# Performance work log

Hardware: AMD Instinct MI355X
Metric: run time of the kernel (lower is better)

The kernel has to match this reference:

```python
import jax, jax.numpy as jnp
import numpy as np
from jax import lax

NUM_COLS = 4
NUM_ROWS = 4
C = 16          # in_channels
K = 3           # kernel_size
B, H, Wd = 8, 128, 128
W_SCALE = 0.05  # keep activations stable through 16 chained ReLU convs


def setup_inputs() -> dict:
    key = jax.random.key(0)
    k1, k2 = jax.random.split(key, 2)
    x = jax.random.normal(k1, (B, C, H, Wd), dtype=jnp.float32)
    # one conv per grid cell: 3 input slots (left/below-prev/above), 3 output streams (right/up/down)
    W = jax.random.normal(k2, (NUM_COLS, NUM_ROWS, 3 * C, 3 * C, K, K), dtype=jnp.float32) * W_SCALE
    b = jnp.zeros((NUM_COLS, NUM_ROWS, 3 * C), dtype=jnp.float32)
    return {"input_tensor": x, "W": W, "b": b}


def _cell(w, bias, ins):
    # ins: list of 1..3 tensors [B, C, H, W]; zero-pad missing slots to 3*C channels
    if len(ins) < 3:
        pad_shape = (ins[0].shape[0], (3 - len(ins)) * C) + ins[0].shape[2:]
        ins = ins + [jnp.zeros(pad_shape, dtype=ins[0].dtype)]
    x = jnp.concatenate(ins, axis=1)  # [B, 3C, H, W]
    y = lax.conv_general_dilated(
        x, w, window_strides=(1, 1), padding="SAME",
        dimension_numbers=("NCHW", "OIHW", "NCHW"))
    y = jax.nn.relu(y + bias[None, :, None, None])
    right, up, down = jnp.split(y, 3, axis=1)  # each [B, C, H, W]
    return (right, up, down)


def reference(input_tensor, W, b):
    # Wavefront sweep: columns left->right, rows top->bottom.
    # outs[row] holds the (right, up, down) tuple of the most recently computed
    # cell in that row (previous column until overwritten this column).
    outs = [None] * NUM_ROWS
    for col in range(NUM_COLS):
        for row in range(NUM_ROWS):
            if col == 0:
                ins = [input_tensor] if row == 0 else [outs[row - 1][-1]]
            else:
                if row == 0:
                    ins = [outs[row][0], outs[row + 1][1]]
                elif row == NUM_ROWS - 1:
                    ins = [outs[row][0], outs[row - 1][-1]]
                else:
                    ins = [outs[row][0], outs[row + 1][1], outs[row - 1][-1]]
            outs[row] = _cell(W[col, row], b[col, row], ins)
    return outs[-1][0]
```

## Files before the change

### kernel.cpp

```cpp
#include <hip/hip_runtime.h>

#define HW    128
#define PW    130
#define NCELL 16
#define ABUF_PER_CELL 23040
#define ABUF_TOTAL (NCELL * ABUF_PER_CELL)
#define NSTREAMS 15
#define BORDER_PX 516
#define BORDER_TASKS (NSTREAMS * 8 * BORDER_PX * 2)

typedef _Float16 half8 __attribute__((ext_vector_type(8)));
typedef _Float16 half4 __attribute__((ext_vector_type(4)));
typedef float    f32x4 __attribute__((ext_vector_type(4)));

#define GLD_LDS(gp, lp) __builtin_amdgcn_global_load_lds( \
    (const __attribute__((address_space(1))) void*)(gp),  \
    (__attribute__((address_space(3))) void*)(lp), 16, 0, 0)

__global__ void prep_w_border_k(const float* __restrict__ W,
                                _Float16* __restrict__ Abuf,
                                _Float16* __restrict__ sbase) {
    int idx = blockIdx.x * 256 + threadIdx.x;
    if (idx < ABUF_TOTAL) {
        int j = idx & 7;
        int t = idx >> 3;
        int co = t % 48;   t /= 48;
        int quad = t & 3;  t >>= 2;
        int chunk = t % 5; t /= 5;
        int slot = t % 3;  t /= 3;
        int cell = t;
        int g = chunk * 4 + quad;
        float v = 0.f;
        if (g < 18) {
            int kh = g / 6, r6 = g % 6;
            int kw = r6 >> 1, cg = r6 & 1;
            int ci = slot * 16 + cg * 8 + j;
            v = W[((size_t)(cell * 48 + co) * 48 + ci) * 9 + kh * 3 + kw];
        }
        Abuf[idx] = (_Float16)v;
        return;
    }
    int t = idx - ABUF_TOTAL;
    if (t >= BORDER_TASKS) return;
    int h  = t & 1;
    int pb = t >> 1;
    int p  = pb % BORDER_PX;
    int bb = pb / BORDER_PX;
    int y, x;
    if (p < 260) {
        y = (p < 130) ? 0 : (PW - 1);
        x = p - ((p < 130) ? 0 : 130);
    } else {
        int e = p - 260;
        y = 1 + (e >> 1);
        x = (e & 1) ? (PW - 1) : 0;
    }
    half8 z = {};
    *(half8*)(sbase + (size_t)bb * (PW * PW * 16)
              + ((size_t)y * PW + x) * 16 + h * 8) = z;
}

struct CellIO {
    const _Float16* in0; const _Float16* in1; const _Float16* in2;
    const _Float16* Ac; const float* bc;
    _Float16* o0; _Float16* o1; _Float16* o2;
    float* fout;
};

template<int LIVE, int NIN, bool FIN, bool XIN>
__device__ __forceinline__ void cell_body(const CellIO& P, int b, _Float16* xh,
                                          const float* xsrc)
{
    const int tid = threadIdx.x;
    const int bx = blockIdx.x, by = blockIdx.y;
    const int x0 = bx * 16, y0 = by * 16;
    const int lane = tid & 63, wv = tid >> 6;
    const int n = lane & 15, quad = lane >> 4;
    const int py0 = wv * 4;

    if constexpr (XIN) {
        for (int task = tid; task < 288; task += 256) {
            int ci = task / 18, iy = task - (task / 18) * 18;
            float v[18];
#pragma unroll
            for (int ix = 0; ix < 18; ++ix) v[ix] = 0.f;
            int gy = y0 + iy - 1;
            if ((unsigned)gy < (unsigned)HW) {
                const float* rp = xsrc + (((size_t)b * 16 + ci) * HW + gy) * HW + x0;
                f32x4 q0 = *(const f32x4*)(rp);
                f32x4 q1 = *(const f32x4*)(rp + 4);
                f32x4 q2 = *(const f32x4*)(rp + 8);
                f32x4 q3 = *(const f32x4*)(rp + 12);
#pragma unroll
                for (int j = 0; j < 4; ++j) {
                    v[1 + j] = q0[j]; v[5 + j] = q1[j];
                    v[9 + j] = q2[j]; v[13 + j] = q3[j];
                }
                if (x0 > 0)       v[0]  = rp[-1];
                if (x0 < HW - 16) v[17] = rp[16];
            }
            int cg = ci >> 3, cj = ci & 7;
#pragma unroll
            for (int ix = 0; ix < 18; ++ix)
                xh[(((iy * 2 + cg) * 18) + ix) * 8 + cj] = (_Float16)v[ix];
        }
    } else {
        const _Float16* const ins[3] = {P.in0, P.in1, P.in2};
#pragma unroll
        for (int s = 0; s < NIN; ++s) {
            const _Float16* src = ins[s] + (size_t)b * (PW * PW * 16)
                                 + ((size_t)(by * 16) * PW + bx * 16) * 16;
            _Float16* base = xh + s * 5184;
            for (int k = wv; k < 10; k += 4) {
                int u = k * 64 + lane;
                int iy = u / 36, r36 = u - iy * 36;
                int cg = r36 / 18, ix = r36 - cg * 18;
                GLD_LDS(src + (iy * PW + ix) * 16 + cg * 8, base + k * 512);
            }
            if (wv == 2 && lane < 8) {
                int u = 640 + lane;
                int ix = u - 630;
                *(half8*)(base + u * 8) =
                    *(const half8*)(src + (17 * PW + ix) * 16 + 8);
            }
        }
    }
    __syncthreads();

    int base_c[5];
#pragma unroll
    for (int c = 0; c < 5; ++c) {
        int g = c * 4 + quad;
        if (g >= 18) g = 0;
        int kh = g / 6, r6 = g % 6;
        int kw = r6 >> 1, cg = r6 & 1;
        base_c[c] = ((py0 + kh) * 2 + cg) * 18 + n + kw;
    }

    f32x4 acc[3][4];
#pragma unroll
    for (int cot = 0; cot < 3; ++cot) {
        if (!(LIVE & (1 << cot))) continue;
#pragma unroll
        for (int r = 0; r < 4; ++r) {
            float bv = P.bc[cot * 16 + quad * 4 + r];
#pragma unroll
            for (int nt = 0; nt < 4; ++nt) acc[cot][nt][r] = bv;
        }
    }

#pragma unroll
    for (int s = 0; s < NIN; ++s) {
        const _Float16* sxh = xh + s * 5184;
        const _Float16* As = P.Ac + (size_t)(s * 5) * 1536 + quad * 384 + n * 8;
#pragma unroll
        for (int c = 0; c < 5; ++c) {
            half8 Bh[4];
#pragma unroll
            for (int nt = 0; nt < 4; ++nt)
                Bh[nt] = *(const half8*)(sxh + (base_c[c] + nt * 36) * 8);
            const _Float16* Ab = As + (size_t)c * 1536;
#pragma unroll
            for (int cot = 0; cot < 3; ++cot) {
                if (!(LIVE & (1 << cot))) continue;
                half8 ah = *(const half8*)(Ab + cot * 128);
#pragma unroll
                for (int nt = 0; nt < 4; ++nt)
                    acc[cot][nt] = __builtin_amdgcn_mfma_f32_16x16x32_f16(ah, Bh[nt], acc[cot][nt], 0, 0, 0);
            }
        }
    }

    if constexpr (FIN) {
#pragma unroll
        for (int nt = 0; nt < 4; ++nt) {
            int y = y0 + py0 + nt, xg = x0 + n;
#pragma unroll
            for (int r = 0; r < 4; ++r) {
                float vv = acc[0][nt][r];
                P.fout[(((size_t)b * 16 + quad * 4 + r) * HW + y) * HW + xg] = vv > 0.f ? vv : 0.f;
            }
        }
    } else {
        _Float16* const outs[3] = {P.o0, P.o1, P.o2};
#pragma unroll
        for (int cot = 0; cot < 3; ++cot) {
            if (!(LIVE & (1 << cot))) continue;
            _Float16* op = outs[cot] + (size_t)b * (PW * PW * 16);
#pragma unroll
            for (int nt = 0; nt < 4; ++nt) {
                int y = y0 + py0 + nt;
                half4 hv;
#pragma unroll
                for (int r = 0; r < 4; ++r) {
                    float vv = acc[cot][nt][r];
                    hv[r] = (_Float16)(vv > 0.f ? vv : 0.f);
                }
                *(half4*)(op + ((size_t)(y + 1) * PW + x0 + n + 1) * 16 + quad * 4) = hv;
            }
        }
    }
}

template<int L0, int N0, int L1, int N1, bool FIN, bool XIN>
__global__ __launch_bounds__(256, 4) void cell_k(CellIO P0, CellIO P1,
                                                 const float* xsrc) {
    constexpr int MAXN = (N0 > N1) ? N0 : N1;
    __shared__ __align__(16) _Float16 xh[MAXN * 5184];
    int b = blockIdx.z & 7;
    if constexpr (L1 > 0) {
        if (blockIdx.z >= 8) { cell_body<L1, N1, false, false>(P1, b, xh, nullptr); return; }
    }
    cell_body<L0, N0, FIN, XIN>(P0, b, xh, xsrc);
}

extern "C" void kernel_launch(void* const* d_in, const int* in_sizes, int n_in,
                              void* d_out, int out_size, void* d_ws, size_t ws_size,
                              hipStream_t stream) {
    const float* x  = (const float*)d_in[0];
    const float* W  = (const float*)d_in[1];
    const float* bi = (const float*)d_in[2];
    float* out = (float*)d_out;

    _Float16* Abuf = (_Float16*)d_ws;
    const size_t abytes = (size_t)NCELL * ABUF_PER_CELL * 2;
    _Float16* q = (_Float16*)((char*)d_ws + abytes);
    _Float16* sbase = q;
    const size_t S = (size_t)8 * PW * PW * 16;

    _Float16 *R[2][4], *U[4], *D[2][2];
    for (int pa = 0; pa < 2; ++pa)
        for (int r = 0; r < 4; ++r) { R[pa][r] = q; q += S; }
    U[0] = nullptr;
    for (int r = 1; r < 4; ++r) { U[r] = q; q += S; }
    D[0][0] = q; q += S; D[0][1] = q; q += S;
    D[1][0] = q; q += S; D[1][1] = q; q += S;

    hipLaunchKernelGGL(prep_w_border_k,
                       dim3((ABUF_TOTAL + BORDER_TASKS + 255) / 256),
                       dim3(256), 0, stream, W, Abuf, sbase);

    auto mkio = [&](int c, int r) -> CellIO {
        CellIO io{};
        if (c == 0) {
            io.in0 = (r == 0) ? nullptr : D[0][(r - 1) & 1];
        } else {
            io.in0 = R[(c - 1) & 1][r];
            if (r == 0)      io.in1 = U[1];
            else if (r == 3) io.in1 = D[c & 1][0];
            else { io.in1 = U[r + 1]; io.in2 = D[c & 1][(r - 1) & 1]; }
        }
        if (c < 3) {
            io.o0 = R[c & 1][r];
            if (r > 0) io.o1 = U[r];
            if (r < 3) io.o2 = D[c & 1][r & 1];
        } else {
            if (r < 3) io.o2 = D[1][r & 1];
            else       io.fout = out;
        }
        io.Ac = Abuf + (size_t)(c * 4 + r) * ABUF_PER_CELL;
        io.bc = bi + (size_t)(c * 4 + r) * 48;
        return io;
    };

    dim3 blk(256), g1(8, 8, 8), g2(8, 8, 16);
#define ONEX(c, r)       do { CellIO a = mkio(c, r); \
    hipLaunchKernelGGL((cell_k<5, 1, 0, 0, false, true>), g1, blk, 0, stream, a, a, x); } while (0)
#define ONE(L, N, c, r)  do { CellIO a = mkio(c, r); \
    hipLaunchKernelGGL((cell_k<L, N, 0, 0, false, false>), g1, blk, 0, stream, a, a, x); } while (0)
#define ONEF(c, r)       do { CellIO a = mkio(c, r); \
    hipLaunchKernelGGL((cell_k<1, 2, 0, 0, true, false>), g1, blk, 0, stream, a, a, x); } while (0)
#define TWO(L0, N0, c0, r0, L1, N1, c1, r1) do { \
    CellIO a = mkio(c0, r0), bb2 = mkio(c1, r1); \
    hipLaunchKernelGGL((cell_k<L0, N0, L1, N1, false, false>), g2, blk, 0, stream, a, bb2, x); } while (0)

    ONEX(0, 0);
    ONE(7, 1, 0, 1);
    TWO(7, 1, 0, 2,  5, 2, 1, 0);
    TWO(3, 1, 0, 3,  7, 3, 1, 1);
    TWO(7, 3, 1, 2,  5, 2, 2, 0);
    TWO(3, 2, 1, 3,  7, 3, 2, 1);
    TWO(7, 3, 2, 2,  4, 2, 3, 0);
    TWO(3, 2, 2, 3,  4, 3, 3, 1);
    ONE(4, 3, 3, 2);
    ONEF(3, 3);
#undef ONEX
#undef ONE
#undef ONEF
#undef TWO
}
```

Measured before the change: 190.0 us.

## Overlap first input-slot compute with remaining slot loads via partial vmcnt waits

For multi-input cells, the first slot's halo tile is staged into LDS and then waited on alone, using a partial vmcnt wait and a raw barrier. The other slots' global-to-LDS loads stay in flight while slot 0's MFMAs run, with a full barrier before slot 1. Bias and the first weight fragments are prefetched into registers before issuing the later loads. The LDS slot is padded so the stray eighth-lane load becomes a uniform 11th wave chunk. The hand-counted vmcnt values must match the issued load counts exactly, and the extra prefetched registers add pressure against the 4-block occupancy target.

Result: no change. 186.9 us (-1.6%).

```diff
diff --git a/kernel.cpp b/kernel.cpp
--- a/kernel.cpp
+++ b/kernel.cpp
@@ -8,6 +8,7 @@
 #define NSTREAMS 15
 #define BORDER_PX 516
 #define BORDER_TASKS (NSTREAMS * 8 * BORDER_PX * 2)
+#define SLOT 5632
 
 typedef _Float16 half8 __attribute__((ext_vector_type(8)));
 typedef _Float16 half4 __attribute__((ext_vector_type(4)));
@@ -78,6 +79,9 @@
     const int n = lane & 15, quad = lane >> 4;
     const int py0 = wv * 4;
 
+    float bv[3][4];
+    half8 a0[3][3];
+
     if constexpr (XIN) {
         for (int task = tid; task < 288; task += 256) {
             int ci = task / 18, iy = task - (task / 18) * 18;
@@ -104,28 +108,52 @@
             for (int ix = 0; ix < 18; ++ix)
                 xh[(((iy * 2 + cg) * 18) + ix) * 8 + cj] = (_Float16)v[ix];
         }
+        __syncthreads();
     } else {
         const _Float16* const ins[3] = {P.in0, P.in1, P.in2};
-#pragma unroll
-        for (int s = 0; s < NIN; ++s) {
+        auto stage = [&](int s) {
             const _Float16* src = ins[s] + (size_t)b * (PW * PW * 16)
                                  + ((size_t)(by * 16) * PW + bx * 16) * 16;
-            _Float16* base = xh + s * 5184;
-            for (int k = wv; k < 10; k += 4) {
-                int u = k * 64 + lane;
-                int iy = u / 36, r36 = u - iy * 36;
-                int cg = r36 / 18, ix = r36 - cg * 18;
-                GLD_LDS(src + (iy * PW + ix) * 16 + cg * 8, base + k * 512);
-            }
-            if (wv == 2 && lane < 8) {
-                int u = 640 + lane;
-                int ix = u - 630;
-                *(half8*)(base + u * 8) =
-                    *(const half8*)(src + (17 * PW + ix) * 16 + 8);
-            }
-        }
-    }
-    __syncthreads();
+            _Float16* base = xh + s * SLOT;
+#pragma unroll
+            for (int k = 0; k < 3; ++k) {
+                int kk = wv + k * 4;
+                if (kk < 11) {
+                    int u = kk * 64 + lane;
+                    int iy = u / 36, r36 = u - iy * 36;
+                    int cg = r36 / 18, ix = r36 - cg * 18;
+                    GLD_LDS(src + (iy * PW + ix) * 16 + cg * 8, base + kk * 512);
+                }
+            }
+        };
+        stage(0);
+        if constexpr (NIN >= 2) {
+            asm volatile("" ::: "memory");
+#pragma unroll
+            for (int cot = 0; cot < 3; ++cot) {
+                if (!(LIVE & (1 << cot))) continue;
+#pragma unroll
+                for (int r = 0; r < 4; ++r) bv[cot][r] = P.bc[cot * 16 + quad * 4 + r];
+            }
+            const _Float16* As0 = P.Ac + quad * 384 + n * 8;
+#pragma unroll
+            for (int c = 0; c < 3; ++c)
+#pragma unroll
+                for (int cot = 0; cot < 3; ++cot) {
+                    if (!(LIVE & (1 << cot))) continue;
+                    a0[c][cot] = *(const half8*)(As0 + c * 1536 + cot * 128);
+                }
+            asm volatile("" ::: "memory");
+#pragma unroll
+            for (int s = 1; s < NIN; ++s) stage(s);
+            if (wv == 3) asm volatile("s_waitcnt vmcnt(%0)" :: "n"((NIN - 1) * 2) : "memory");
+            else         asm volatile("s_waitcnt vmcnt(%0)" :: "n"((NIN - 1) * 3) : "memory");
+            __builtin_amdgcn_s_barrier();
+            asm volatile("" ::: "memory");
+        } else {
+            __syncthreads();
+        }
+    }
 
     int base_c[5];
 #pragma unroll
@@ -137,21 +165,23 @@
         base_c[c] = ((py0 + kh) * 2 + cg) * 18 + n + kw;
     }
 
+    constexpr bool PIPE = (!XIN) && (NIN >= 2);
     f32x4 acc[3][4];
 #pragma unroll
     for (int cot = 0; cot < 3; ++cot) {
         if (!(LIVE & (1 << cot))) continue;
 #pragma unroll
         for (int r = 0; r < 4; ++r) {
-            float bv = P.bc[cot * 16 + quad * 4 + r];
-#pragma unroll
-            for (int nt = 0; nt < 4; ++nt) acc[cot][nt][r] = bv;
+            float bvv = PIPE ? bv[cot][r] : P.bc[cot * 16 + quad * 4 + r];
+#pragma unroll
+            for (int nt = 0; nt < 4; ++nt) acc[cot][nt][r] = bvv;
         }
     }
 
 #pragma unroll
     for (int s = 0; s < NIN; ++s) {
-        const _Float16* sxh = xh + s * 5184;
+        if (PIPE && s == 1) __syncthreads();
+        const _Float16* sxh = xh + s * SLOT;
         const _Float16* As = P.Ac + (size_t)(s * 5) * 1536 + quad * 384 + n * 8;
 #pragma unroll
         for (int c = 0; c < 5; ++c) {
@@ -163,7 +193,13 @@
 #pragma unroll
             for (int cot = 0; cot < 3; ++cot) {
                 if (!(LIVE & (1 << cot))) continue;
-                half8 ah = *(const half8*)(Ab + cot * 128);
+                half8 ah;
+                if constexpr (PIPE) {
+                    if (s == 0 && c < 3) ah = a0[c][cot];
+                    else                 ah = *(const half8*)(Ab + cot * 128);
+                } else {
+                    ah = *(const half8*)(Ab + cot * 128);
+                }
 #pragma unroll
                 for (int nt = 0; nt < 4; ++nt)
                     acc[cot][nt] = __builtin_amdgcn_mfma_f32_16x16x32_f16(ah, Bh[nt], acc[cot][nt], 0, 0, 0);
@@ -206,7 +242,7 @@
 __global__ __launch_bounds__(256, 4) void cell_k(CellIO P0, CellIO P1,
                                                  const float* xsrc) {
     constexpr int MAXN = (N0 > N1) ? N0 : N1;
-    __shared__ __align__(16) _Float16 xh[MAXN * 5184];
+    __shared__ __align__(16) _Float16 xh[MAXN * SLOT];
     int b = blockIdx.z & 7;
     if constexpr (L1 > 0) {
         if (blockIdx.z >= 8) { cell_body<L1, N1, false, false>(P1, b, xh, nullptr); return; }
```
